# Kernel optimization log

Hardware: AMD Instinct MI355X
Metric: run time of the kernel (lower is better)

Reference implementation:

```python
import jax, jax.numpy as jnp
import numpy as np
import math

B, N, D, L, H, FF, T = 8, 256, 384, 6, 8, 1536, 4
Dh = D // H  # 48, divisible by 6 for 3D rotary
N_M1 = T + 1 + 2 * N  # learn tokens + state + hand + head
S = 2 * N_M1


def rotary_pe_3d(x, coords):
    # x: [B,H,S,Dh], coords: [B,S,3]. Split head dim into 3 axis chunks,
    # apply standard RoPE per axis using the continuous coordinate as position.
    dh = x.shape[-1]
    d = dh // 3
    half = d // 2
    inv_freq = 1.0 / (10000.0 ** (jnp.arange(half, dtype=x.dtype) / half))
    outs = []
    for a in range(3):
        xa = x[..., a * d:(a + 1) * d]
        ang = coords[..., a][:, None, :, None] * inv_freq  # [B,1,S,half]
        c, s = jnp.cos(ang), jnp.sin(ang)
        x1, x2 = xa[..., :half], xa[..., half:]
        outs.append(jnp.concatenate([x1 * c - x2 * s, x1 * s + x2 * c], axis=-1))
    return jnp.concatenate(outs, axis=-1)


def layernorm(x, g, b):
    m = jnp.mean(x, axis=-1, keepdims=True)
    v = jnp.var(x, axis=-1, keepdims=True)
    return (x - m) * jax.lax.rsqrt(v + 1e-5) * g + b


def transformer_layer(src, coords_src, mask, Wq, bq, Wk, bk, Wv, bv, Wo, bo, W1, b1, W2, b2, g1, be1, g2, be2):
    Bsz, Ss, _ = src.shape
    q = jnp.einsum('bsd,od->bso', src, Wq) + bq
    k = jnp.einsum('bsd,od->bso', src, Wk) + bk
    v = jnp.einsum('bsd,od->bso', src, Wv) + bv
    q = q.reshape(Bsz, Ss, H, Dh).transpose(0, 2, 1, 3)
    k = k.reshape(Bsz, Ss, H, Dh).transpose(0, 2, 1, 3)
    v = v.reshape(Bsz, Ss, H, Dh).transpose(0, 2, 1, 3)
    q = rotary_pe_3d(q, coords_src)
    k = rotary_pe_3d(k, coords_src)
    scores = jnp.einsum('bhqd,bhkd->bhqk', q, k) / math.sqrt(Dh)
    scores = jnp.where(mask[None, None, :, :], -jnp.inf, scores)
    attn = jnp.einsum('bhqk,bhkd->bhqd', jax.nn.softmax(scores, axis=-1), v)
    attn = attn.transpose(0, 2, 1, 3).reshape(Bsz, Ss, D)
    attn = jnp.einsum('bsd,od->bso', attn, Wo) + bo
    src2 = layernorm(src + attn, g1, be1)
    ff = jnp.einsum('bsf,of->bso', jax.nn.gelu(jnp.einsum('bsd,fd->bsf', src2, W1) + b1, approximate=False), W2) + b2
    return layernorm(src2 + ff, g2, be2)


def setup_inputs() -> dict:
    key = jax.random.key(0)
    ks = jax.random.split(key, 32)
    rnd = lambda i, shape, scale=1.0: (jax.random.normal(ks[i], shape, dtype=jnp.float32) * scale)
    inp = {
        'hand_token_t': rnd(0, (B, N, D)),
        'head_token_t': rnd(1, (B, N, D)),
        'hand_token_m1': rnd(2, (B, N, D)),
        'head_token_m1': rnd(3, (B, N, D)),
        'coords_hand_t': rnd(4, (B, N, 3)),
        'coords_head_t': rnd(5, (B, N, 3)),
        'coords_hand_m1': rnd(6, (B, N, 3)),
        'coords_head_m1': rnd(7, (B, N, 3)),
        'state_t': rnd(8, (B, D)),
        'state_m1': rnd(9, (B, D)),
        'trans_head_t': rnd(10, (B, 3)),
        'trans_head_m1': rnd(11, (B, 3)),
        'tokens_m1': rnd(12, (1, T, D), 0.02),
        'tokens_t': rnd(13, (1, T, D), 0.02),
        'Wq': rnd(14, (L, D, D), 0.02), 'bq': jnp.zeros((L, D), jnp.float32),
        'Wk': rnd(15, (L, D, D), 0.02), 'bk': jnp.zeros((L, D), jnp.float32),
        'Wv': rnd(16, (L, D, D), 0.02), 'bv': jnp.zeros((L, D), jnp.float32),
        'Wo': rnd(17, (L, D, D), 0.02), 'bo': jnp.zeros((L, D), jnp.float32),
        'W1': rnd(18, (L, FF, D), 0.02), 'b1': jnp.zeros((L, FF), jnp.float32),
        'W2': rnd(19, (L, D, FF), 0.02), 'b2': jnp.zeros((L, D), jnp.float32),
        'g1': jnp.ones((L, D), jnp.float32), 'be1': jnp.zeros((L, D), jnp.float32),
        'g2': jnp.ones((L, D), jnp.float32), 'be2': jnp.zeros((L, D), jnp.float32),
    }
    return inp


def reference(hand_token_t, head_token_t, hand_token_m1, head_token_m1,
              coords_hand_t, coords_head_t, coords_hand_m1, coords_head_m1,
              state_t, state_m1, trans_head_t, trans_head_m1,
              tokens_m1, tokens_t, Wq, bq, Wk, bk, Wv, bv, Wo, bo,
              W1, b1, W2, b2, g1, be1, g2, be2):
    # Build token sequence: [state_m1, hand_m1, head_m1, learn_m1, state_t, hand_t, head_t, learn_t]
    tok_m1 = jnp.broadcast_to(tokens_m1, (B, T, D))
    tok_t = jnp.broadcast_to(tokens_t, (B, T, D))
    coord_m1 = jnp.broadcast_to(trans_head_m1[:, None, :], (B, T, 3))
    coord_t = jnp.broadcast_to(trans_head_t[:, None, :], (B, T, 3))
    src = jnp.concatenate([
        state_m1[:, None, :], hand_token_m1, head_token_m1, tok_m1,
        state_t[:, None, :], hand_token_t, head_token_t, tok_t], axis=1)
    coords_src = jnp.concatenate([
        trans_head_m1[:, None, :], coords_hand_m1, coords_head_m1, coord_m1,
        trans_head_t[:, None, :], coords_hand_t, coords_head_t, coord_t], axis=1)
    # block-causal mask: m1 block cannot attend to t block
    mask = jnp.zeros((S, S), dtype=bool).at[:N_M1, N_M1:].set(True)
    for i in range(L):
        src = transformer_layer(src, coords_src, mask,
                                Wq[i], bq[i], Wk[i], bk[i], Wv[i], bv[i], Wo[i], bo[i],
                                W1[i], b1[i], W2[i], b2[i], g1[i], be1[i], g2[i], be2[i])
    return src[:, -T:, :]
```

## Files before the change

kernel.cpp:

```cpp
#include <hip/hip_runtime.h>
#include <hip/hip_bf16.h>
#include <math.h>

#define BB 8
#define NN 256
#define DD 384
#define LL 6
#define HH 8
#define FFD 1536
#define TT 4
#define DH 48
#define NM1 517
#define SS 1034
#define SSP 1088
#define MROWS (BB*SS)
#define NQKV 1152
#define QSCALE 0.14433756729740643f

typedef unsigned short u16;
typedef unsigned int u32;
typedef short bf8 __attribute__((ext_vector_type(8)));
typedef float f32x4 __attribute__((ext_vector_type(4)));

__device__ __forceinline__ u16 f2bf(float f) {
  __hip_bfloat16 h = __float2bfloat16(f);
  return *reinterpret_cast<u16*>(&h);
}
__device__ __forceinline__ float bf2f(u16 u) {
  __hip_bfloat16 h;
  *reinterpret_cast<u16*>(&h) = u;
  return __bfloat162float(h);
}
__device__ __forceinline__ void async16(void* lds, const void* g) {
  __builtin_amdgcn_global_load_lds(
      (const __attribute__((address_space(1))) unsigned int*)g,
      (__attribute__((address_space(3))) unsigned int*)lds, 16, 0, 0);
}

__global__ void build_src(const float* __restrict__ hand_t, const float* __restrict__ head_t,
                          const float* __restrict__ hand_m1, const float* __restrict__ head_m1,
                          const float* __restrict__ state_t, const float* __restrict__ state_m1,
                          const float* __restrict__ tok_m1, const float* __restrict__ tok_t,
                          float* __restrict__ src, u16* __restrict__ srcb) {
  int idx = blockIdx.x * 256 + threadIdx.x;
  if (idx >= BB * SS * DD) return;
  int d = idx % DD;
  int bs = idx / DD;
  int s = bs % SS;
  int b = bs / SS;
  float val;
  if (s == 0)               val = state_m1[b * DD + d];
  else if (s <= NN)         val = hand_m1[((size_t)(b * NN + (s - 1))) * DD + d];
  else if (s <= 2 * NN)     val = head_m1[((size_t)(b * NN + (s - 1 - NN))) * DD + d];
  else if (s <= 2 * NN + TT) val = tok_m1[(s - (2 * NN + 1)) * DD + d];
  else if (s == NM1)        val = state_t[b * DD + d];
  else if (s <= NM1 + NN)   val = hand_t[((size_t)(b * NN + (s - NM1 - 1))) * DD + d];
  else if (s <= NM1 + 2 * NN) val = head_t[((size_t)(b * NN + (s - NM1 - 1 - NN))) * DD + d];
  else                      val = tok_t[(s - (NM1 + 2 * NN + 1)) * DD + d];
  src[idx] = val;
  srcb[idx] = f2bf(val);
}

__global__ void build_coords(const float* __restrict__ c_hand_t, const float* __restrict__ c_head_t,
                             const float* __restrict__ c_hand_m1, const float* __restrict__ c_head_m1,
                             const float* __restrict__ tr_t, const float* __restrict__ tr_m1,
                             float* __restrict__ coords) {
  int idx = blockIdx.x * 256 + threadIdx.x;
  if (idx >= BB * SS * 3) return;
  int a = idx % 3;
  int bs = idx / 3;
  int s = bs % SS;
  int b = bs / SS;
  float val;
  if (s == 0)               val = tr_m1[b * 3 + a];
  else if (s <= NN)         val = c_hand_m1[(b * NN + (s - 1)) * 3 + a];
  else if (s <= 2 * NN)     val = c_head_m1[(b * NN + (s - 1 - NN)) * 3 + a];
  else if (s <= 2 * NN + TT) val = tr_m1[b * 3 + a];
  else if (s == NM1)        val = tr_t[b * 3 + a];
  else if (s <= NM1 + NN)   val = c_hand_t[(b * NN + (s - NM1 - 1)) * 3 + a];
  else if (s <= NM1 + 2 * NN) val = c_head_t[(b * NN + (s - NM1 - 1 - NN)) * 3 + a];
  else                      val = tr_t[b * 3 + a];
  coords[idx] = val;
}

__global__ void build_trig(const float* __restrict__ coords, float2* __restrict__ trig) {
  int idx = blockIdx.x * 256 + threadIdx.x;
  if (idx >= BB * SS * 24) return;
  int i = idx & 7;
  int axis = (idx >> 3) % 3;
  int bs = idx / 24;
  float cv = coords[bs * 3 + axis];
  float inv = expf(-(float)i * 1.1512925464970229f);
  float ang = cv * inv;
  trig[idx] = make_float2(cosf(ang), sinf(ang));
}

__global__ void cvt_bf(const float* __restrict__ in, u16* __restrict__ out, int n4) {
  int idx = blockIdx.x * 256 + threadIdx.x;
  if (idx >= n4) return;
  float4 v = reinterpret_cast<const float4*>(in)[idx];
  short4 o;
  o.x = (short)f2bf(v.x); o.y = (short)f2bf(v.y);
  o.z = (short)f2bf(v.z); o.w = (short)f2bf(v.w);
  reinterpret_cast<short4*>(out)[idx] = o;
}

__global__ void pack_qkv(const float* __restrict__ Wq, const float* __restrict__ Wk,
                         const float* __restrict__ Wv, u16* __restrict__ wqkv) {
  int idx = blockIdx.x * 256 + threadIdx.x;
  const int TOTAL = LL * NQKV * 96;
  if (idx >= TOTAL) return;
  int k4 = idx % 96;
  int n = (idx / 96) % NQKV;
  int l = idx / (96 * NQKV);
  int sel = n / 384, nn = n - sel * 384;
  const float* W = (sel == 0) ? Wq : ((sel == 1) ? Wk : Wv);
  float4 v = *reinterpret_cast<const float4*>(W + ((size_t)l * 384 + nn) * 384 + k4 * 4);
  short4 o;
  o.x = (short)f2bf(v.x); o.y = (short)f2bf(v.y);
  o.z = (short)f2bf(v.z); o.w = (short)f2bf(v.w);
  *reinterpret_cast<short4*>(wqkv + ((size_t)(l * NQKV + n) * 384 + k4 * 4)) = o;
}

__global__ void pack_bqkv(const float* __restrict__ bq, const float* __restrict__ bk,
                          const float* __restrict__ bv, float* __restrict__ bqkv) {
  int idx = blockIdx.x * 256 + threadIdx.x;
  if (idx >= LL * NQKV) return;
  int n = idx % NQKV, l = idx / NQKV;
  int sel = n / 384, nn = n - sel * 384;
  const float* Bp = (sel == 0) ? bq : ((sel == 1) ? bk : bv);
  bqkv[idx] = Bp[l * 384 + nn];
}

__global__ void pad_vt(u16* __restrict__ vt) {
  int idx = blockIdx.x * 256 + threadIdx.x;
  const int PADW = SSP - SS;
  if (idx >= 64 * DH * PADW) return;
  int c = idx % PADW;
  int rd = idx / PADW;
  vt[(size_t)rd * SSP + SS + c] = 0;
}

__global__ void pad_qk(u16* __restrict__ qh, u16* __restrict__ kh) {
  int idx = blockIdx.x * 256 + threadIdx.x;
  if (idx >= 64 * SS * 16) return;
  int c = idx & 15;
  int row = idx >> 4;
  qh[(size_t)row * 64 + 48 + c] = 0;
  kh[(size_t)row * 64 + 48 + c] = 0;
}

template <int EPI, int OUT>
__global__ __launch_bounds__(512) void gemm_as(
    const u16* __restrict__ Ab, const u16* __restrict__ Wb,
    const float* __restrict__ bias, const float2* __restrict__ trig,
    const float* __restrict__ Rf,
    float* __restrict__ Cf, u16* __restrict__ Cb,
    u16* __restrict__ Ck, u16* __restrict__ Cv,
    int M, int N, int K) {
  constexpr int BUFSZ = 24576;
  __shared__ __align__(16) char sm[2 * BUFSZ];
  const int tid = threadIdx.x;

  const int nxt = N >> 6;
  const int Mt = (M + 127) >> 7;
  const int gL = blockIdx.x;
  const int x8 = gL & 7, jj = gL >> 3;
  const int mt_ = x8 * 9 + jj / nxt;
  if (mt_ >= Mt) return;
  const int bm = mt_ << 7, bn = (jj % nxt) << 6;

  const int lid = tid & 63, w = tid >> 6;
  const int wm = w >> 1, wn = w & 1;
  const int l15 = lid & 15, lg = lid >> 4;
  const int lr = lid >> 3, lu = lid & 7;
  const int swz = lu ^ lr;
  f32x4 acc[2][2] = {};

  auto stage = [&](int bsel, int k0) {
    char* base = sm + bsel * BUFSZ;
#pragma unroll
    for (int q = 0; q < 2; ++q) {
      int row = w * 16 + q * 8 + lr;
      int grow = bm + row; if (grow >= M) grow = M - 1;
      async16(base + w * 2048 + q * 1024, Ab + (size_t)grow * K + k0 + (swz << 3));
    }
    async16(base + 16384 + w * 1024, Wb + (size_t)(bn + w * 8 + lr) * K + k0 + (swz << 3));
  };

  stage(0, 0);
  int bs = 0;

  for (int k0 = 0; k0 < K; k0 += 64) {
    if (k0 + 64 < K) {
      stage(bs ^ 1, k0 + 64);
      asm volatile("s_waitcnt vmcnt(3)" ::: "memory");
    } else {
      asm volatile("s_waitcnt vmcnt(0)" ::: "memory");
    }
    __builtin_amdgcn_s_barrier();
    const char* base = sm + bs * BUFSZ;
    bf8 a[2][2], bfr[2][2];
#pragma unroll
    for (int kf = 0; kf < 2; ++kf) {
#pragma unroll
      for (int mt = 0; mt < 2; ++mt) {
        int row = wm * 32 + mt * 16 + l15;
        int off = ((row << 7) + (kf << 6) + (lg << 4)) ^ ((row & 7) << 4);
        a[kf][mt] = *reinterpret_cast<const bf8*>(base + off);
      }
#pragma unroll
      for (int nt = 0; nt < 2; ++nt) {
        int row = wn * 32 + nt * 16 + l15;
        int off = 16384 + (((row << 7) + (kf << 6) + (lg << 4)) ^ ((row & 7) << 4));
        bfr[kf][nt] = *reinterpret_cast<const bf8*>(base + off);
      }
    }
#pragma unroll
    for (int kf = 0; kf < 2; ++kf)
#pragma unroll
      for (int mt = 0; mt < 2; ++mt)
#pragma unroll
        for (int nt = 0; nt < 2; ++nt)
          acc[mt][nt] = __builtin_amdgcn_mfma_f32_16x16x32_bf16(a[kf][mt], bfr[kf][nt], acc[mt][nt], 0, 0, 0);
    asm volatile("s_waitcnt lgkmcnt(0)" ::: "memory");
    __builtin_amdgcn_s_barrier();
    bs ^= 1;
  }

  if constexpr (OUT != 2) {
#pragma unroll
    for (int nt = 0; nt < 2; ++nt) {
      const int n = bn + wn * 32 + nt * 16 + l15;
      const float bsv = bias[n];
#pragma unroll
      for (int mt = 0; mt < 2; ++mt) {
        const int m0 = bm + wm * 32 + mt * 16 + lg * 4;
#pragma unroll
        for (int r = 0; r < 4; ++r) {
          int m = m0 + r;
          if (m >= M) continue;
          float v = acc[mt][nt][r] + bsv;
          if (EPI == 1) v = 0.5f * v * (1.0f + erff(v * 0.70710678118654752f));
          if (OUT == 0) Cf[(size_t)m * N + n] = v + Rf[(size_t)m * N + n];
          else          Cb[(size_t)m * N + n] = f2bf(v);
        }
      }
    }
  } else {
    float* tile = (float*)sm;
#pragma unroll
    for (int nt = 0; nt < 2; ++nt) {
      const int nl = wn * 32 + nt * 16 + l15;
      const float bsv = bias[bn + nl];
#pragma unroll
      for (int mt = 0; mt < 2; ++mt) {
#pragma unroll
        for (int r = 0; r < 4; ++r) {
          int ml = wm * 32 + mt * 16 + lg * 4 + r;
          tile[ml * 65 + nl] = acc[mt][nt][r] + bsv;
        }
      }
    }
    __syncthreads();
    const int bnm = bn % 384;
    const int sel = bn / 384;
    if (sel < 2) {
      u16* Cqk = (sel == 0) ? Cb : Ck;
      const int d = lid;
      const int nn_ = bnm + d;
      const int hdiv = nn_ / 48, hrem = nn_ - hdiv * 48;
      const int axis = hrem >> 4, ii = hrem & 7;
      const bool hi = (hrem & 8) != 0;
      for (int si = 0; si < 16; ++si) {
        int row = w * 16 + si;
        int m = bm + row;
        if (m >= M) break;
        int bI = m / SS, s = m - bI * SS;
        float v = tile[row * 65 + d];
        float p = tile[row * 65 + (d ^ 8)];
        float2 t = trig[(size_t)(bI * SS + s) * 24 + axis * 8 + ii];
        float outv = hi ? (p * t.y + v * t.x) : (v * t.x - p * t.y);
        if (sel == 0) outv *= QSCALE;
        Cqk[((size_t)(bI * HH + hdiv) * SS + s) * 64 + hrem] = f2bf(outv);
      }
    } else {
      const int srow = tid & 127, dq = tid >> 7;
      const int m = bm + srow;
      if (m < M) {
        int bI = m / SS, s = m - bI * SS;
        for (int di = 0; di < 16; ++di) {
          int d = dq * 16 + di;
          int nn_ = bnm + d;
          int hdiv = nn_ / 48, hrem = nn_ - hdiv * 48;
          Cv[((size_t)(bI * HH + hdiv) * DH + hrem) * SSP + s] = f2bf(tile[srow * 65 + d]);
        }
      }
    }
  }
}

__global__ __launch_bounds__(256) void attn_mfma(const u16* __restrict__ qh,
                                                 const u16* __restrict__ kh,
                                                 const u16* __restrict__ vt,
                                                 u16* __restrict__ outb) {
  __shared__ __align__(16) char sm[28672];
  const int tid = threadIdx.x;
  const int lid = tid & 63, w = tid >> 6;
  const int l15 = lid & 15, lg = lid >> 4;
  const int lr = lid >> 3, lu = lid & 7;
  const int swz8 = (lu ^ lr) << 3;

  const int f = blockIdx.x;
  const int low = f & 7, j = f >> 3;
  const int gi = j / 17, qp17 = j - gi * 17;
  const int g = gi * 8 + low;
  const int h = g & 7, b = g >> 3;
  const int qblk = 16 - qp17;
  const int bh = b * HH + h;
  const int q0w = qblk * 64 + w * 16;
  const u16* kbase = kh + (size_t)bh * SS * 64;
  const u16* vbase = vt + (size_t)bh * DH * SSP;

  bf8 qf[2];
  {
    int row = q0w + l15; if (row >= SS) row = SS - 1;
    const u16* qp = qh + ((size_t)bh * SS + row) * 64;
    qf[0] = *reinterpret_cast<const bf8*>(qp + lg * 8);
    qf[1] = *reinterpret_cast<const bf8*>(qp + 32 + lg * 8);
  }
  const int qrow = q0w + l15;

  float m_q = -1e30f, l_q = 0.f;
  f32x4 accO[3] = {};

  const int nch = (qblk < 8) ? 9 : 17;

  auto stage = [&](int bsel, int c) {
    const int j0 = c * 64;
    char* kb = sm + bsel * 14336;
    char* vb = kb + 8192;
#pragma unroll
    for (int qq = 0; qq < 2; ++qq) {
      int is = w * 2 + qq;
      int s = is * 8 + lr;
      int jt_ = s >> 4, lgs = (s >> 2) & 3, rr = s & 3;
      int p = ((jt_ >> 1) << 5) + (lgs << 3) + ((jt_ & 1) << 2) + rr;
      int jrow = j0 + p; if (jrow >= SS) jrow = SS - 1;
      async16(kb + is * 1024, kbase + (size_t)jrow * 64 + swz8);
    }
    async16(vb + w * 1024, vbase + (size_t)(w * 8 + lr) * SSP + j0 + swz8);
    if (w < 2)
      async16(vb + (4 + w) * 1024, vbase + (size_t)((4 + w) * 8 + lr) * SSP + j0 + swz8);
  };

  stage(0, 0);
  __syncthreads();
  int bsel = 0;

  for (int c = 0; c < nch; ++c) {
    if (c + 1 < nch) stage(bsel ^ 1, c + 1);
    const int j0 = c * 64;
    const char* kb = sm + bsel * 14336;
    const char* vb = kb + 8192;

    f32x4 sv[4];
#pragma unroll
    for (int jt = 0; jt < 4; ++jt) {
      int row = jt * 16 + l15;
      int off0 = ((row << 7) + (lg << 4)) ^ ((row & 7) << 4);
      int off1 = ((row << 7) + 64 + (lg << 4)) ^ ((row & 7) << 4);
      bf8 kb0 = *reinterpret_cast<const bf8*>(kb + off0);
      bf8 kb1 = *reinterpret_cast<const bf8*>(kb + off1);
      f32x4 z = {};
      z = __builtin_amdgcn_mfma_f32_16x16x32_bf16(kb0, qf[0], z, 0, 0, 0);
      z = __builtin_amdgcn_mfma_f32_16x16x32_bf16(kb1, qf[1], z, 0, 0, 0);
      sv[jt] = z;
    }

    const bool domask = (c == 16) | ((q0w < NM1) & (c >= 8));
    if (domask) {
#pragma unroll
      for (int jt = 0; jt < 4; ++jt)
#pragma unroll
        for (int r = 0; r < 4; ++r) {
          int kabs = j0 + ((jt >> 1) << 5) + (lg << 3) + ((jt & 1) << 2) + r;
          if (kabs >= SS || (qrow < NM1 && kabs >= NM1)) sv[jt][r] = -1e30f;
        }
    }

    float mx = sv[0][0];
#pragma unroll
    for (int jt = 0; jt < 4; ++jt)
#pragma unroll
      for (int r = 0; r < 4; ++r) mx = fmaxf(mx, sv[jt][r]);
    mx = fmaxf(mx, __shfl_xor(mx, 16));
    mx = fmaxf(mx, __shfl_xor(mx, 32));

    const bool skip = __all(mx <= m_q);
    const float mn = skip ? m_q : fmaxf(m_q, mx);

    float pv[4][4];
    float ps = 0.f;
#pragma unroll
    for (int jt = 0; jt < 4; ++jt)
#pragma unroll
      for (int r = 0; r < 4; ++r) {
        float p = __expf(sv[jt][r] - mn);
        pv[jt][r] = p;
        ps += p;
      }
    ps += __shfl_xor(ps, 16);
    ps += __shfl_xor(ps, 32);

    if (!skip) {
      float alpha = __expf(m_q - mn);
      l_q = l_q * alpha + ps;
      m_q = mn;
      const int lg4 = lg * 4;
      float a0 = __shfl(alpha, lg4);
      float a1 = __shfl(alpha, lg4 + 1);
      float a2 = __shfl(alpha, lg4 + 2);
      float a3 = __shfl(alpha, lg4 + 3);
#pragma unroll
      for (int dt = 0; dt < 3; ++dt) {
        accO[dt][0] *= a0; accO[dt][1] *= a1;
        accO[dt][2] *= a2; accO[dt][3] *= a3;
      }
    } else {
      l_q += ps;
    }

    bf8 pa[2];
#pragma unroll
    for (int jc = 0; jc < 2; ++jc) {
      u32 w0 = (u32)f2bf(pv[jc * 2][0])     | ((u32)f2bf(pv[jc * 2][1]) << 16);
      u32 w1 = (u32)f2bf(pv[jc * 2][2])     | ((u32)f2bf(pv[jc * 2][3]) << 16);
      u32 w2 = (u32)f2bf(pv[jc * 2 + 1][0]) | ((u32)f2bf(pv[jc * 2 + 1][1]) << 16);
      u32 w3 = (u32)f2bf(pv[jc * 2 + 1][2]) | ((u32)f2bf(pv[jc * 2 + 1][3]) << 16);
      uint4 t = make_uint4(w0, w1, w2, w3);
      pa[jc] = *reinterpret_cast<bf8*>(&t);
    }

#pragma unroll
    for (int dt = 0; dt < 3; ++dt) {
      int row = dt * 16 + l15;
#pragma unroll
      for (int jc = 0; jc < 2; ++jc) {
        int off = ((row << 7) + (jc << 6) + (lg << 4)) ^ ((row & 7) << 4);
        bf8 vb8 = *reinterpret_cast<const bf8*>(vb + off);
        accO[dt] = __builtin_amdgcn_mfma_f32_16x16x32_bf16(pa[jc], vb8, accO[dt], 0, 0, 0);
      }
    }
    __syncthreads();
    bsel ^= 1;
  }

  float linv = 1.0f / l_q;
  const int lg4 = lg * 4;
  float il[4];
#pragma unroll
  for (int r = 0; r < 4; ++r) il[r] = __shfl(linv, lg4 + r);
#pragma unroll
  for (int r = 0; r < 4; ++r) {
    int q = q0w + lg4 + r;
    if (q >= SS) continue;
#pragma unroll
    for (int dt = 0; dt < 3; ++dt) {
      int d = dt * 16 + l15;
      outb[((size_t)(b * SS + q)) * DD + h * DH + d] = f2bf(accO[dt][r] * il[r]);
    }
  }
}

__global__ __launch_bounds__(128) void add_ln(const float* __restrict__ a,
                                              const float* __restrict__ g,
                                              const float* __restrict__ be,
                                              float* __restrict__ out,
                                              u16* __restrict__ outb) {
  __shared__ float p1[2], p2[2];
  const int row = blockIdx.x;
  const int t = threadIdx.x;
  const size_t base = (size_t)row * DD;
  float x0 = a[base + t];
  float x1 = a[base + t + 128];
  float x2 = a[base + t + 256];
  float s = x0 + x1 + x2;
#pragma unroll
  for (int off = 32; off; off >>= 1) s += __shfl_xor(s, off);
  if ((t & 63) == 0) p1[t >> 6] = s;
  __syncthreads();
  float mean = (p1[0] + p1[1]) * (1.0f / 384.0f);
  float d0 = x0 - mean, d1 = x1 - mean, d2 = x2 - mean;
  float vsum = d0 * d0 + d1 * d1 + d2 * d2;
#pragma unroll
  for (int off = 32; off; off >>= 1) vsum += __shfl_xor(vsum, off);
  if ((t & 63) == 0) p2[t >> 6] = vsum;
  __syncthreads();
  float var = (p2[0] + p2[1]) * (1.0f / 384.0f);
  float rs = rsqrtf(var + 1e-5f);
  float o0 = d0 * rs * g[t]       + be[t];
  float o1 = d1 * rs * g[t + 128] + be[t + 128];
  float o2 = d2 * rs * g[t + 256] + be[t + 256];
  out[base + t] = o0;        outb[base + t] = f2bf(o0);
  out[base + t + 128] = o1;  outb[base + t + 128] = f2bf(o1);
  out[base + t + 256] = o2;  outb[base + t + 256] = f2bf(o2);
}

__global__ void copy_out(const float* __restrict__ src, float* __restrict__ out) {
  int idx = blockIdx.x * 256 + threadIdx.x;
  if (idx >= BB * TT * DD) return;
  int d = idx % DD;
  int bt = idx / DD;
  int t = bt % TT;
  int b = bt / TT;
  out[idx] = src[((size_t)b * SS + (SS - TT) + t) * DD + d];
}

extern "C" void kernel_launch(void* const* d_in, const int* in_sizes, int n_in,
                              void* d_out, int out_size, void* d_ws, size_t ws_size,
                              hipStream_t stream) {
  const float* hand_t    = (const float*)d_in[0];
  const float* head_t    = (const float*)d_in[1];
  const float* hand_m1   = (const float*)d_in[2];
  const float* head_m1   = (const float*)d_in[3];
  const float* c_hand_t  = (const float*)d_in[4];
  const float* c_head_t  = (const float*)d_in[5];
  const float* c_hand_m1 = (const float*)d_in[6];
  const float* c_head_m1 = (const float*)d_in[7];
  const float* state_t   = (const float*)d_in[8];
  const float* state_m1  = (const float*)d_in[9];
  const float* tr_t      = (const float*)d_in[10];
  const float* tr_m1     = (const float*)d_in[11];
  const float* tok_m1    = (const float*)d_in[12];
  const float* tok_t     = (const float*)d_in[13];
  const float* Wq = (const float*)d_in[14];
  const float* bq = (const float*)d_in[15];
  const float* Wk = (const float*)d_in[16];
  const float* bk = (const float*)d_in[17];
  const float* Wv = (const float*)d_in[18];
  const float* bv = (const float*)d_in[19];
  const float* Wo = (const float*)d_in[20];
  const float* bo = (const float*)d_in[21];
  const float* W1 = (const float*)d_in[22];
  const float* b1 = (const float*)d_in[23];
  const float* W2 = (const float*)d_in[24];
  const float* b2 = (const float*)d_in[25];
  const float* g1 = (const float*)d_in[26];
  const float* be1 = (const float*)d_in[27];
  const float* g2 = (const float*)d_in[28];
  const float* be2 = (const float*)d_in[29];

  const size_t SRC_N = (size_t)BB * SS * DD;
  float* src    = (float*)d_ws;
  float* src2   = src + SRC_N;
  float* bufB   = src2 + SRC_N;
  float* coords = bufB + SRC_N;
  float* bqkv   = coords + (size_t)BB * SS * 3;
  float2* trig  = (float2*)(bqkv + (size_t)LL * NQKV);
  u16* srcb  = (u16*)(trig + (size_t)BB * SS * 24);
  u16* src2b = srcb + SRC_N;
  u16* attnb = src2b + SRC_N;
  u16* qh  = attnb + SRC_N;
  const size_t QH_N = (size_t)BB * HH * SS * 64;
  u16* khb = qh + QH_N;
  u16* vtb = khb + QH_N;
  u16* hbf = vtb + (size_t)64 * DH * SSP;
  u16* wqkv_b = hbf + (size_t)MROWS * FFD;
  const size_t WD = (size_t)LL * DD * DD;
  const size_t WF = (size_t)LL * FFD * DD;
  u16* wo_bf = wqkv_b + (size_t)LL * NQKV * 384;
  u16* w1_bf = wo_bf + WD;
  u16* w2_bf = w1_bf + WF;

  const int M = MROWS;
  dim3 blk(256);
  dim3 blk512(512);

  build_src<<<(BB * SS * DD + 255) / 256, blk, 0, stream>>>(
      hand_t, head_t, hand_m1, head_m1, state_t, state_m1, tok_m1, tok_t, src, srcb);
  build_coords<<<(BB * SS * 3 + 255) / 256, blk, 0, stream>>>(
      c_hand_t, c_head_t, c_hand_m1, c_head_m1, tr_t, tr_m1, coords);
  build_trig<<<(BB * SS * 24 + 255) / 256, blk, 0, stream>>>(coords, trig);
  pack_qkv<<<(LL * NQKV * 96 + 255) / 256, blk, 0, stream>>>(Wq, Wk, Wv, wqkv_b);
  pack_bqkv<<<(LL * NQKV + 255) / 256, blk, 0, stream>>>(bq, bk, bv, bqkv);
  cvt_bf<<<(int)(WD / 4 + 255) / 256, blk, 0, stream>>>(Wo, wo_bf, (int)(WD / 4));
  cvt_bf<<<(int)(WF / 4 + 255) / 256, blk, 0, stream>>>(W1, w1_bf, (int)(WF / 4));
  cvt_bf<<<(int)(WF / 4 + 255) / 256, blk, 0, stream>>>(W2, w2_bf, (int)(WF / 4));
  pad_vt<<<(64 * DH * (SSP - SS) + 255) / 256, blk, 0, stream>>>(vtb);
  pad_qk<<<(64 * SS * 16 + 255) / 256, blk, 0, stream>>>(qh, khb);

  dim3 gqkv(18 * 72);
  dim3 gwo(6 * 72);
  dim3 gf1(24 * 72);
  dim3 gf2(6 * 72);
  dim3 gattn(17 * 8 * 8);

  for (int l = 0; l < LL; ++l) {
    const u16* Wqkv_l = wqkv_b + (size_t)l * NQKV * 384;
    const u16* Wo_l = wo_bf + (size_t)l * DD * DD;
    const u16* W1_l = w1_bf + (size_t)l * FFD * DD;
    const u16* W2_l = w2_bf + (size_t)l * DD * FFD;

    gemm_as<0, 2><<<gqkv, blk512, 0, stream>>>(srcb, Wqkv_l, bqkv + l * NQKV, trig,
                                               nullptr, nullptr, qh, khb, vtb, M, NQKV, DD);
    attn_mfma<<<gattn, blk, 0, stream>>>(qh, khb, vtb, attnb);
    gemm_as<0, 0><<<gwo, blk512, 0, stream>>>(attnb, Wo_l, bo + l * DD, nullptr,
                                              src, bufB, nullptr, nullptr, nullptr, M, DD, DD);
    add_ln<<<M, 128, 0, stream>>>(bufB, g1 + l * DD, be1 + l * DD, src2, src2b);
    gemm_as<1, 1><<<gf1, blk512, 0, stream>>>(src2b, W1_l, b1 + l * FFD, nullptr,
                                              nullptr, nullptr, hbf, nullptr, nullptr, M, FFD, DD);
    gemm_as<0, 0><<<gf2, blk512, 0, stream>>>(hbf, W2_l, b2 + l * DD, nullptr,
                                              src2, bufB, nullptr, nullptr, nullptr, M, DD, FFD);
    add_ln<<<M, 128, 0, stream>>>(bufB, g2 + l * DD, be2 + l * DD, src, srcb);
  }
  copy_out<<<(BB * TT * DD + 255) / 256, blk, 0, stream>>>(src, (float*)d_out);
}
```

Before: 903.6 us.

## Tune attention softmax and sync, pack four rows per layernorm block

Folds log2(e) into the Q scale so the softmax can use the native exp2 instruction. Replaces __syncthreads in the attention loop with explicit vmcnt/lgkmcnt waits plus raw barriers, so the next K/V chunk prefetch stays in flight. Adds s_setprio around the MFMA sections and a max3-style reduction. add_ln now handles four rows per 512-thread block, cutting block count. The vmcnt(3) count depends on the exact number of async loads each thread issues, and a wrong count risks races.

```diff
diff --git a/kernel.cpp b/kernel.cpp
--- a/kernel.cpp
+++ b/kernel.cpp
@@ -15,7 +15,7 @@
 #define SSP 1088
 #define MROWS (BB*SS)
 #define NQKV 1152
-#define QSCALE 0.14433756729740643f
+#define QSCALE2 (0.14433756729740643f * 1.4426950408889634f)
 
 typedef unsigned short u16;
 typedef unsigned int u32;
@@ -30,6 +30,9 @@
   __hip_bfloat16 h;
   *reinterpret_cast<u16*>(&h) = u;
   return __bfloat162float(h);
+}
+__device__ __forceinline__ float max3f(float a, float b, float c) {
+  return fmaxf(fmaxf(a, b), c);
 }
 __device__ __forceinline__ void async16(void* lds, const void* g) {
   __builtin_amdgcn_global_load_lds(
@@ -281,7 +284,7 @@
         float p = tile[row * 65 + (d ^ 8)];
         float2 t = trig[(size_t)(bI * SS + s) * 24 + axis * 8 + ii];
         float outv = hi ? (p * t.y + v * t.x) : (v * t.x - p * t.y);
-        if (sel == 0) outv *= QSCALE;
+        if (sel == 0) outv *= QSCALE2;
         Cqk[((size_t)(bI * HH + hdiv) * SS + s) * 64 + hrem] = f2bf(outv);
       }
     } else {
@@ -359,12 +362,19 @@
   int bsel = 0;
 
   for (int c = 0; c < nch; ++c) {
-    if (c + 1 < nch) stage(bsel ^ 1, c + 1);
+    if (c + 1 < nch) {
+      stage(bsel ^ 1, c + 1);
+      asm volatile("s_waitcnt vmcnt(3)" ::: "memory");
+    } else {
+      asm volatile("s_waitcnt vmcnt(0)" ::: "memory");
+    }
+    __builtin_amdgcn_s_barrier();
     const int j0 = c * 64;
     const char* kb = sm + bsel * 14336;
     const char* vb = kb + 8192;
 
     f32x4 sv[4];
+    __builtin_amdgcn_s_setprio(1);
 #pragma unroll
     for (int jt = 0; jt < 4; ++jt) {
       int row = jt * 16 + l15;
@@ -377,6 +387,7 @@
       z = __builtin_amdgcn_mfma_f32_16x16x32_bf16(kb1, qf[1], z, 0, 0, 0);
       sv[jt] = z;
     }
+    __builtin_amdgcn_s_setprio(0);
 
     const bool domask = (c == 16) | ((q0w < NM1) & (c >= 8));
     if (domask) {
@@ -389,11 +400,14 @@
         }
     }
 
-    float mx = sv[0][0];
-#pragma unroll
-    for (int jt = 0; jt < 4; ++jt)
-#pragma unroll
-      for (int r = 0; r < 4; ++r) mx = fmaxf(mx, sv[jt][r]);
+    float mx = max3f(sv[0][0], sv[0][1], sv[0][2]);
+    mx = max3f(mx, sv[0][3], sv[1][0]);
+    mx = max3f(mx, sv[1][1], sv[1][2]);
+    mx = max3f(mx, sv[1][3], sv[2][0]);
+    mx = max3f(mx, sv[2][1], sv[2][2]);
+    mx = max3f(mx, sv[2][3], sv[3][0]);
+    mx = max3f(mx, sv[3][1], sv[3][2]);
+    mx = fmaxf(mx, sv[3][3]);
     mx = fmaxf(mx, __shfl_xor(mx, 16));
     mx = fmaxf(mx, __shfl_xor(mx, 32));
 
@@ -406,7 +420,7 @@
     for (int jt = 0; jt < 4; ++jt)
 #pragma unroll
       for (int r = 0; r < 4; ++r) {
-        float p = __expf(sv[jt][r] - mn);
+        float p = __builtin_amdgcn_exp2f(sv[jt][r] - mn);
         pv[jt][r] = p;
         ps += p;
       }
@@ -414,7 +428,7 @@
     ps += __shfl_xor(ps, 32);
 
     if (!skip) {
-      float alpha = __expf(m_q - mn);
+      float alpha = __builtin_amdgcn_exp2f(m_q - mn);
       l_q = l_q * alpha + ps;
       m_q = mn;
       const int lg4 = lg * 4;
@@ -442,6 +456,7 @@
       pa[jc] = *reinterpret_cast<bf8*>(&t);
     }
 
+    __builtin_amdgcn_s_setprio(1);
 #pragma unroll
     for (int dt = 0; dt < 3; ++dt) {
       int row = dt * 16 + l15;
@@ -452,7 +467,9 @@
         accO[dt] = __builtin_amdgcn_mfma_f32_16x16x32_bf16(pa[jc], vb8, accO[dt], 0, 0, 0);
       }
     }
-    __syncthreads();
+    __builtin_amdgcn_s_setprio(0);
+    asm volatile("s_waitcnt lgkmcnt(0)" ::: "memory");
+    __builtin_amdgcn_s_barrier();
     bsel ^= 1;
   }
 
@@ -473,14 +490,15 @@
   }
 }
 
-__global__ __launch_bounds__(128) void add_ln(const float* __restrict__ a,
+__global__ __launch_bounds__(512) void add_ln(const float* __restrict__ a,
                                               const float* __restrict__ g,
                                               const float* __restrict__ be,
                                               float* __restrict__ out,
                                               u16* __restrict__ outb) {
-  __shared__ float p1[2], p2[2];
-  const int row = blockIdx.x;
-  const int t = threadIdx.x;
+  __shared__ float p1[4][2], p2[4][2];
+  const int rl = threadIdx.x >> 7;
+  const int t = threadIdx.x & 127;
+  const int row = blockIdx.x * 4 + rl;
   const size_t base = (size_t)row * DD;
   float x0 = a[base + t];
   float x1 = a[base + t + 128];
@@ -488,16 +506,16 @@
   float s = x0 + x1 + x2;
 #pragma unroll
   for (int off = 32; off; off >>= 1) s += __shfl_xor(s, off);
-  if ((t & 63) == 0) p1[t >> 6] = s;
+  if ((t & 63) == 0) p1[rl][t >> 6] = s;
   __syncthreads();
-  float mean = (p1[0] + p1[1]) * (1.0f / 384.0f);
+  float mean = (p1[rl][0] + p1[rl][1]) * (1.0f / 384.0f);
   float d0 = x0 - mean, d1 = x1 - mean, d2 = x2 - mean;
   float vsum = d0 * d0 + d1 * d1 + d2 * d2;
 #pragma unroll
   for (int off = 32; off; off >>= 1) vsum += __shfl_xor(vsum, off);
-  if ((t & 63) == 0) p2[t >> 6] = vsum;
+  if ((t & 63) == 0) p2[rl][t >> 6] = vsum;
   __syncthreads();
-  float var = (p2[0] + p2[1]) * (1.0f / 384.0f);
+  float var = (p2[rl][0] + p2[rl][1]) * (1.0f / 384.0f);
   float rs = rsqrtf(var + 1e-5f);
   float o0 = d0 * rs * g[t]       + be[t];
   float o1 = d1 * rs * g[t + 128] + be[t + 128];
@@ -607,12 +625,12 @@
     attn_mfma<<<gattn, blk, 0, stream>>>(qh, khb, vtb, attnb);
     gemm_as<0, 0><<<gwo, blk512, 0, stream>>>(attnb, Wo_l, bo + l * DD, nullptr,
                                               src, bufB, nullptr, nullptr, nullptr, M, DD, DD);
-    add_ln<<<M, 128, 0, stream>>>(bufB, g1 + l * DD, be1 + l * DD, src2, src2b);
+    add_ln<<<M / 4, blk512, 0, stream>>>(bufB, g1 + l * DD, be1 + l * DD, src2, src2b);
     gemm_as<1, 1><<<gf1, blk512, 0, stream>>>(src2b, W1_l, b1 + l * FFD, nullptr,
                                               nullptr, nullptr, hbf, nullptr, nullptr, M, FFD, DD);
     gemm_as<0, 0><<<gf2, blk512, 0, stream>>>(hbf, W2_l, b2 + l * DD, nullptr,
                                               src2, bufB, nullptr, nullptr, nullptr, M, DD, FFD);
-    add_ln<<<M, 128, 0, stream>>>(bufB, g2 + l * DD, be2 + l * DD, src, srcb);
+    add_ln<<<M / 4, blk512, 0, stream>>>(bufB, g2 + l * DD, be2 + l * DD, src, srcb);
   }
   copy_out<<<(BB * TT * DD + 255) / 256, blk, 0, stream>>>(src, (float*)d_out);
 }
```

New measurement: 906.5 us. Within noise of the previous version (+0.3%).
